# Optimization experiments

Measured on AMD Instinct MI355X. Metric: run time of the kernel, lower is better.

Reference implementation:

```python
import jax, jax.numpy as jnp
import numpy as np

_LOG2PI = 0.9189385332046727
_NUM_VARS = 256   # D
_NUM_UNITS = 64   # K
_BATCH = 2048     # B
_NUM_LEVELS = 8   # log2(D)


def setup_inputs() -> dict:
    key = jax.random.key(0)
    D, K, B = _NUM_VARS, _NUM_UNITS, _BATCH
    inp = {}
    inp["x"] = jax.random.normal(jax.random.fold_in(key, 0), (B, 1, D), dtype=jnp.float32)
    inp["mu"] = jax.random.normal(jax.random.fold_in(key, 1), (D, K), dtype=jnp.float32)
    inp["log_sigma"] = 0.1 * jax.random.normal(jax.random.fold_in(key, 2), (D, K), dtype=jnp.float32)
    # input-layer bookkeeping: each fold reads one (permuted) variable of x
    inp["in_scope_idx"] = jax.random.permutation(jax.random.fold_in(key, 3), D)[:, None]
    F = D
    for l in range(1, _NUM_LEVELS + 1):
        # fold bookkeeping: irregular pairing of previous-layer folds (permutation -> valid partition)
        inp[f"fold_idx{l}"] = jax.random.permutation(jax.random.fold_in(key, 10 + l), F).reshape(F // 2, 2)
        F //= 2
        inp[f"w{l}"] = jax.random.normal(jax.random.fold_in(key, 100 + l), (F, K, K), dtype=jnp.float32)
    return inp


def _circuit(x, mu, log_sigma, ws, in_scope_idx, fold_idxs):
    # input layer gather: x (B,C,D) -> x[..., idx] (B,C,F,s) -> permute (F,C,B,s)
    xg = jnp.transpose(x[..., in_scope_idx], (2, 1, 0, 3))  # (D,1,B,1)
    xv = xg[:, 0, :, 0]  # (D,B): C=1, scope size 1
    # Gaussian input layer, log densities: (F=D, B, K)
    z = (xv[:, :, None] - mu[:, None, :]) * jnp.exp(-log_sigma)[:, None, :]
    out = -0.5 * z * z - log_sigma[:, None, :] - _LOG2PI
    for fidx, w in zip(fold_idxs, ws):
        # folded Hadamard product layer: gather (F,2,B,K) via bookkeeping, add in log-space
        h = out[fidx].sum(axis=1)  # (F,B,K)
        # folded dense sum layer: y[f,b,j] = logsumexp_k( log softmax(w)[f,j,k] + h[f,b,k] )
        wp = jax.nn.softmax(w, axis=-1)  # (F,K,K)
        m = jnp.max(h, axis=-1, keepdims=True)
        out = jnp.log(jnp.einsum('fbk,fjk->fbj', jnp.exp(h - m), wp)) + m  # (F,B,K)
    # final bookkeeping: (F_out=1, B, K) -> transpose(0,1) -> (B, 1, K)
    return jnp.transpose(out, (1, 0, 2))


def reference(x, mu, log_sigma, w1, w2, w3, w4, w5, w6, w7, w8,
              in_scope_idx, fold_idx1, fold_idx2, fold_idx3, fold_idx4,
              fold_idx5, fold_idx6, fold_idx7, fold_idx8):
    ws = (w1, w2, w3, w4, w5, w6, w7, w8)
    fold_idxs = (fold_idx1, fold_idx2, fold_idx3, fold_idx4,
                 fold_idx5, fold_idx6, fold_idx7, fold_idx8)
    return _circuit(x, mu, log_sigma, ws, in_scope_idx, fold_idxs)
```

## Files before the change

kernel.cpp:

```cpp
#include <hip/hip_runtime.h>
#include <math.h>

#define LOG2PI_F  0.9189385332046727f
#define INV_LN2_F 1.4426950408889634f
#define LN2_F     0.6931471805599453f
#define SROW      72

typedef short bf16x8 __attribute__((ext_vector_type(8)));
typedef float f32x4  __attribute__((ext_vector_type(4)));

struct __align__(16) Op { int w; int c0; int c1; int pad; };

#define WS_WBJ   0u
#define WS_A     2097152u
#define WS_B     2162688u
#define WS_C     2228224u
#define WS_XT    2293760u
#define WS_SCHED 4390912u
#define WS_L4A   4395008u
#define WS_L4M   8589312u

__device__ __forceinline__ short bfr(float f) {
    unsigned int u = __float_as_uint(f);
    u += 0x7fffu + ((u >> 16) & 1u);
    return (short)(u >> 16);
}

__device__ __forceinline__ unsigned pk2(float a, float b) {
    return (unsigned)(unsigned short)bfr(a) | ((unsigned)(unsigned short)bfr(b) << 16);
}

struct F8v { float v[8]; };
__device__ __forceinline__ F8v ld8(const float* p) {
    F8v r;
    float4 a = *(const float4*)p;
    float4 b = *(const float4*)(p + 4);
    r.v[0]=a.x; r.v[1]=a.y; r.v[2]=a.z; r.v[3]=a.w;
    r.v[4]=b.x; r.v[5]=b.y; r.v[6]=b.z; r.v[7]=b.w;
    return r;
}

__device__ __forceinline__ void up8(int4 v, float* o) {
    o[0] = __uint_as_float(((unsigned)v.x) << 16);
    o[1] = __uint_as_float(((unsigned)v.x) & 0xffff0000u);
    o[2] = __uint_as_float(((unsigned)v.y) << 16);
    o[3] = __uint_as_float(((unsigned)v.y) & 0xffff0000u);
    o[4] = __uint_as_float(((unsigned)v.z) << 16);
    o[5] = __uint_as_float(((unsigned)v.z) & 0xffff0000u);
    o[6] = __uint_as_float(((unsigned)v.w) << 16);
    o[7] = __uint_as_float(((unsigned)v.w) & 0xffff0000u);
}

__device__ __forceinline__ float rmax16(const float hv[16]) {
    float m01 = fmaxf(hv[0], hv[1]),  m23 = fmaxf(hv[2], hv[3]);
    float m45 = fmaxf(hv[4], hv[5]),  m67 = fmaxf(hv[6], hv[7]);
    float m89 = fmaxf(hv[8], hv[9]),  mab = fmaxf(hv[10], hv[11]);
    float mcd = fmaxf(hv[12], hv[13]), mef = fmaxf(hv[14], hv[15]);
    float hm = fmaxf(fmaxf(fmaxf(m01, m23), fmaxf(m45, m67)),
                     fmaxf(fmaxf(m89, mab), fmaxf(mcd, mef)));
    hm = fmaxf(hm, __shfl_xor(hm, 16, 64));
    hm = fmaxf(hm, __shfl_xor(hm, 32, 64));
    return hm;
}

__device__ __forceinline__ void pack_p(const float e[16], bf16x8& a0, bf16x8& a1) {
    int4 p0, p1;
    p0.x = __builtin_amdgcn_perm(__float_as_uint(e[1]),  __float_as_uint(e[0]),  0x07060302u);
    p0.y = __builtin_amdgcn_perm(__float_as_uint(e[3]),  __float_as_uint(e[2]),  0x07060302u);
    p0.z = __builtin_amdgcn_perm(__float_as_uint(e[5]),  __float_as_uint(e[4]),  0x07060302u);
    p0.w = __builtin_amdgcn_perm(__float_as_uint(e[7]),  __float_as_uint(e[6]),  0x07060302u);
    p1.x = __builtin_amdgcn_perm(__float_as_uint(e[9]),  __float_as_uint(e[8]),  0x07060302u);
    p1.y = __builtin_amdgcn_perm(__float_as_uint(e[11]), __float_as_uint(e[10]), 0x07060302u);
    p1.z = __builtin_amdgcn_perm(__float_as_uint(e[13]), __float_as_uint(e[12]), 0x07060302u);
    p1.w = __builtin_amdgcn_perm(__float_as_uint(e[15]), __float_as_uint(e[14]), 0x07060302u);
    a0 = *(bf16x8*)&p0;
    a1 = *(bf16x8*)&p1;
}

__global__ __launch_bounds__(256) void prep_kernel(
    const float* __restrict__ w1, const float* __restrict__ w2,
    const float* __restrict__ w3, const float* __restrict__ w4,
    const float* __restrict__ w5, const float* __restrict__ w6,
    const float* __restrict__ w7, const float* __restrict__ w8,
    const float* __restrict__ mu, const float* __restrict__ ls,
    const float* __restrict__ x,  const int* __restrict__ scope,
    const int* __restrict__ f1, const int* __restrict__ f2,
    const int* __restrict__ f3, const int* __restrict__ f4,
    const int* __restrict__ f5, const int* __restrict__ f6,
    const int* __restrict__ f7, const int* __restrict__ f8,
    char* __restrict__ ws)
{
    const int bx = blockIdx.x, t = threadIdx.x;
    if (bx < 255) {
        const int g = bx;
        const float* src;
        if (g < 128)      src = w1 + g * 4096;
        else if (g < 192) src = w2 + (g - 128) * 4096;
        else if (g < 224) src = w3 + (g - 192) * 4096;
        else if (g < 240) src = w4 + (g - 224) * 4096;
        else if (g < 248) src = w5 + (g - 240) * 4096;
        else if (g < 252) src = w6 + (g - 248) * 4096;
        else              src = (g < 254) ? (w7 + (g - 252) * 4096) : w8;

        const int row = t >> 2;
        const int sub = t & 3;
        const float* rp = src + row * 64 + sub * 16;
        float4 v0 = *(const float4*)rp;
        float4 v1 = *(const float4*)(rp + 4);
        float4 v2 = *(const float4*)(rp + 8);
        float4 v3 = *(const float4*)(rp + 12);
        float v[16] = { v0.x, v0.y, v0.z, v0.w,  v1.x, v1.y, v1.z, v1.w,
                        v2.x, v2.y, v2.z, v2.w,  v3.x, v3.y, v3.z, v3.w };
        float mx = fmaxf(fmaxf(fmaxf(fmaxf(v[0], v[1]), fmaxf(v[2], v[3])),
                               fmaxf(fmaxf(v[4], v[5]), fmaxf(v[6], v[7]))),
                         fmaxf(fmaxf(fmaxf(v[8], v[9]), fmaxf(v[10], v[11])),
                               fmaxf(fmaxf(v[12], v[13]), fmaxf(v[14], v[15]))));
        mx = fmaxf(mx, __shfl_xor(mx, 1, 64));
        mx = fmaxf(mx, __shfl_xor(mx, 2, 64));
        float e[16], sm = 0.f;
        #pragma unroll
        for (int i = 0; i < 16; ++i) { e[i] = __expf(v[i] - mx); sm += e[i]; }
        sm += __shfl_xor(sm, 1, 64);
        sm += __shfl_xor(sm, 2, 64);
        const float inv = 1.0f / sm;

        unsigned short* dst = (unsigned short*)(ws + WS_WBJ) + g * 4096;
        #pragma unroll
        for (int c = 0; c < 2; ++c) {
            const int tc = 2 * sub + c;
            const int f  = ((row >> 4) << 1) | (tc >> 2);
            const int ln = ((tc & 3) << 4) | (row & 15);
            int4 pk;
            pk.x = (int)pk2(e[c*8+0] * inv, e[c*8+1] * inv);
            pk.y = (int)pk2(e[c*8+2] * inv, e[c*8+3] * inv);
            pk.z = (int)pk2(e[c*8+4] * inv, e[c*8+5] * inv);
            pk.w = (int)pk2(e[c*8+6] * inv, e[c*8+7] * inv);
            *(int4*)(dst + (size_t)(f * 64 + ln) * 8) = pk;
        }
    } else if (bx < 319) {
        const int idx = (bx - 255) * 256 + t;
        float m = mu[idx], l = ls[idx];
        float is2 = __expf(-2.0f * l);
        ((float*)(ws + WS_A))[idx] = -0.5f * is2 * INV_LN2_F;
        ((float*)(ws + WS_B))[idx] = m * is2 * INV_LN2_F;
        ((float*)(ws + WS_C))[idx] = (-0.5f * m * m * is2 - l - LOG2PI_F) * INV_LN2_F;
    } else if (bx < 575) {
        const int bb = bx - 319;
        const int sd = scope[t];
        float* xT = (float*)(ws + WS_XT);
        #pragma unroll
        for (int i = 0; i < 8; ++i) {
            int b = bb * 8 + i;
            xT[t * 2048 + b] = x[b * 256 + sd];
        }
    } else {
        __shared__ int sf[512];
        for (int i = t; i < 256; i += 256) sf[i]        = f1[i];
        for (int i = t; i < 128; i += 256) sf[256 + i]  = f2[i];
        for (int i = t; i <  64; i += 256) sf[384 + i]  = f3[i];
        for (int i = t; i <  32; i += 256) sf[448 + i]  = f4[i];
        for (int i = t; i <  16; i += 256) sf[480 + i]  = f5[i];
        for (int i = t; i <   8; i += 256) sf[496 + i]  = f6[i];
        for (int i = t; i <   4; i += 256) sf[504 + i]  = f7[i];
        for (int i = t; i <   2; i += 256) sf[508 + i]  = f8[i];
        __syncthreads();
        const int* F1 = &sf[0];   const int* F2 = &sf[256];
        const int* F3 = &sf[384]; const int* F4 = &sf[448];
        const int* F5 = &sf[480]; const int* F6 = &sf[496];
        const int* F7 = &sf[504]; const int* F8 = &sf[508];
        Op* base = (Op*)(ws + WS_SCHED);
        if (t < 16) {
            Op* o = base + t * 15;
            int r0 = F4[2*t], r1 = F4[2*t+1];
            int P[4] = { F3[2*r0], F3[2*r0+1], F3[2*r1], F3[2*r1+1] };
            #pragma unroll
            for (int j = 0; j < 4; ++j) {
                int L0 = F2[2*P[j]], L1 = F2[2*P[j]+1];
                o[2*j]   = { L0 * 4096, F1[2*L0], F1[2*L0+1], 0 };
                o[2*j+1] = { L1 * 4096, F1[2*L1], F1[2*L1+1], 0 };
                o[8+j]   = { (128 + P[j]) * 4096, 0, 0, 0 };
            }
            o[12] = { (192 + r0) * 4096, 0, 0, 0 };
            o[13] = { (192 + r1) * 4096, 0, 0, 0 };
            o[14] = { (224 + t)  * 4096, 0, 0, 0 };
        } else if (t == 16) {
            Op* o = base + 240;
            int g[4] = { F7[2*F8[0]], F7[2*F8[0]+1], F7[2*F8[1]], F7[2*F8[1]+1] };
            #pragma unroll
            for (int a = 0; a < 4; ++a) {
                int l0 = F6[2*g[a]], l1 = F6[2*g[a]+1];
                o[2*a]   = { (240 + l0) * 4096, F5[2*l0], F5[2*l0+1], 0 };
                o[2*a+1] = { (240 + l1) * 4096, F5[2*l1], F5[2*l1+1], 0 };
                o[8+a]   = { (248 + g[a]) * 4096, 0, 0, 0 };
            }
            o[12] = { (252 + F8[0]) * 4096, 0, 0, 0 };
            o[13] = { (252 + F8[1]) * 4096, 0, 0, 0 };
            o[14] = { 254 * 4096, 0, 0, 0 };
        }
    }
}

__device__ __forceinline__ void load_bfrag(const unsigned short* __restrict__ wbJ,
                                           int w, int lane, int4 bf[8]) {
    const int4* wp = (const int4*)(wbJ + w);
    #pragma unroll
    for (int f = 0; f < 8; ++f) bf[f] = wp[f * 64 + lane];
}

__device__ __forceinline__ void prod_norm(const float av[16], const float bv[16],
                                          float MA, float MB,
                                          float p[16], float& Mrow) {
    float pv[16];
    #pragma unroll
    for (int i = 0; i < 16; ++i) pv[i] = av[i] * bv[i];
    const float rm = rmax16(pv);
    const int e = (int)((__float_as_uint(rm) >> 23) & 0xFF) - 127;
    #pragma unroll
    for (int i = 0; i < 16; ++i) p[i] = ldexpf(pv[i], -e);
    Mrow = MA + MB + (float)e;
}

__device__ __forceinline__ void gauss_p(const Op& op,
    const float* __restrict__ xT, const float* __restrict__ Ag,
    const float* __restrict__ Bg, const float* __restrict__ Cg,
    int rowStart, int m, int q, float p[16], float& Mrow)
{
    const int d0 = op.c0, d1 = op.c1;
    const float xv0 = xT[d0 * 2048 + rowStart + m];
    const float xv1 = xT[d1 * 2048 + rowStart + m];
    const float x0s = xv0 * xv0, x1s = xv1 * xv1;
    float hv[16];
    #pragma unroll
    for (int kh = 0; kh < 2; ++kh) {
        const int kb = kh * 32 + q * 8;
        F8v A0 = ld8(Ag + d0*64 + kb), B0 = ld8(Bg + d0*64 + kb);
        F8v C0 = ld8(Cg + d0*64 + kb);
        F8v A1 = ld8(Ag + d1*64 + kb), B1 = ld8(Bg + d1*64 + kb);
        F8v C1 = ld8(Cg + d1*64 + kb);
        #pragma unroll
        for (int i = 0; i < 8; ++i) {
            float t0 = fmaf(A0.v[i], x0s, C0.v[i]);
            t0 = fmaf(B0.v[i], xv0, t0);
            float t1 = fmaf(A1.v[i], x1s, C1.v[i]);
            t1 = fmaf(B1.v[i], xv1, t1);
            hv[kh*8+i] = t0 + t1;
        }
    }
    const float hm = rmax16(hv);
    #pragma unroll
    for (int i = 0; i < 16; ++i) p[i] = __builtin_amdgcn_exp2f(hv[i] - hm);
    Mrow = hm;
}

__device__ __forceinline__ void gprod_p(const Op& op,
    const unsigned short* __restrict__ inAcc, const float* __restrict__ inM,
    int rowStart, int m, int q, float p[16], float& Mrow)
{
    const int4* A4 = (const int4*)(inAcc + (size_t)(op.c0 * 2048 + rowStart + m) * 64);
    const int4* B4 = (const int4*)(inAcc + (size_t)(op.c1 * 2048 + rowStart + m) * 64);
    float av[16], bv[16];
    up8(A4[q], av); up8(A4[4+q], av + 8);
    up8(B4[q], bv); up8(B4[4+q], bv + 8);
    prod_norm(av, bv, inM[op.c0 * 2048 + rowStart + m],
              inM[op.c1 * 2048 + rowStart + m], p, Mrow);
}

__device__ __forceinline__ void slot_prod(const unsigned short* slotS, const float* Mslot,
                                          int sA, int sB, int rowBase, int m, int q,
                                          float p[16], float& Mrow)
{
    const int4* A4 = (const int4*)(slotS + sA * 32 * SROW + (rowBase + m) * SROW);
    const int4* B4 = (const int4*)(slotS + sB * 32 * SROW + (rowBase + m) * SROW);
    float av[16], bv[16];
    up8(A4[q], av); up8(A4[4+q], av + 8);
    up8(B4[q], bv); up8(B4[4+q], bv + 8);
    prod_norm(av, bv, Mslot[sA * 32 + rowBase + m],
              Mslot[sB * 32 + rowBase + m], p, Mrow);
}

__device__ __forceinline__ void mfma8(const float p[16], const int4 bf[8], f32x4 acc[4]) {
    bf16x8 a0, a1;
    pack_p(p, a0, a1);
    #pragma unroll
    for (int jt = 0; jt < 4; ++jt) {
        f32x4 z = {0.f, 0.f, 0.f, 0.f};
        z = __builtin_amdgcn_mfma_f32_16x16x32_bf16(a0, *(bf16x8*)&bf[jt*2+0], z, 0, 0, 0);
        z = __builtin_amdgcn_mfma_f32_16x16x32_bf16(a1, *(bf16x8*)&bf[jt*2+1], z, 0, 0, 0);
        acc[jt] = z;
    }
}

__device__ __forceinline__ void store_slot(unsigned short* slotS, float* Mslot,
                                           int sl, int rowBase, const f32x4 acc[4],
                                           float Mrow, int m, int q)
{
    unsigned short* S = slotS + sl * 32 * SROW;
    #pragma unroll
    for (int jt = 0; jt < 4; ++jt)
        #pragma unroll
        for (int r = 0; r < 4; ++r)
            S[(rowBase + q*4 + r) * SROW + jt*16 + m] = (unsigned short)bfr(acc[jt][r]);
    if (q == 0) Mslot[sl * 32 + rowBase + m] = Mrow;
}

__device__ __forceinline__ void wave_fence() {
    __builtin_amdgcn_wave_barrier();
    __builtin_amdgcn_s_waitcnt(0xC07F);
    __builtin_amdgcn_wave_barrier();
}

template<int NH>
__device__ __forceinline__ void mix_core(const int4 bf[8],
    unsigned short* slotS, float* Mslot,
    int sA, int sB, int sD, int m, int q)
{
    if constexpr (NH == 2) {
        float p0[16], p1[16], M0, M1;
        slot_prod(slotS, Mslot, sA, sB, 0,  m, q, p0, M0);
        slot_prod(slotS, Mslot, sA, sB, 16, m, q, p1, M1);
        f32x4 acc0[4], acc1[4];
        mfma8(p0, bf, acc0);
        mfma8(p1, bf, acc1);
        store_slot(slotS, Mslot, sD, 0,  acc0, M0, m, q);
        store_slot(slotS, Mslot, sD, 16, acc1, M1, m, q);
    } else {
        float p[16], M;
        slot_prod(slotS, Mslot, sA, sB, 0, m, q, p, M);
        f32x4 acc[4];
        mfma8(p, bf, acc);
        store_slot(slotS, Mslot, sD, 0, acc, M, m, q);
    }
}

template<int MODE>
__global__ __launch_bounds__(256) void circuit_coop(
    const unsigned short* __restrict__ wbJ,
    const Op* __restrict__ schedG, int ntile,
    const float* __restrict__ xT, const float* __restrict__ Ag,
    const float* __restrict__ Bg, const float* __restrict__ Cg,
    const unsigned short* __restrict__ inAcc, const float* __restrict__ inM,
    unsigned short* __restrict__ outAcc, float* __restrict__ outM,
    float* __restrict__ outLog)
{
    constexpr int NH = (MODE == 0) ? 2 : 1;
    __shared__ __align__(16) unsigned short slotS[8 * 32 * SROW];
    __shared__ float Mslot[8 * 32];
    __shared__ Op ops[16];

    const int t    = threadIdx.x;
    const int wv   = t >> 6;
    const int lane = t & 63;
    const int m    = lane & 15;
    const int q    = lane >> 4;
    const int s    = blockIdx.x / ntile;
    const int b0   = (blockIdx.x % ntile) * (16 * NH);

    if (t < 15) *(int4*)&ops[t] = ((const int4*)(schedG + s * 15))[t];
    __syncthreads();

    int4 bf2[8];
    load_bfrag(wbJ, ops[8 + wv].w, lane, bf2);

    #pragma unroll
    for (int i = 0; i < 2; ++i) {
        const int sl = 2 * wv + i;
        const Op op = ops[sl];
        int4 bf[8];
        load_bfrag(wbJ, op.w, lane, bf);
        if constexpr (NH == 2) {
            float p0[16], p1[16], M0, M1;
            if (MODE == 0) {
                gauss_p(op, xT, Ag, Bg, Cg, b0,      m, q, p0, M0);
                gauss_p(op, xT, Ag, Bg, Cg, b0 + 16, m, q, p1, M1);
            } else {
                gprod_p(op, inAcc, inM, b0,      m, q, p0, M0);
                gprod_p(op, inAcc, inM, b0 + 16, m, q, p1, M1);
            }
            f32x4 acc0[4], acc1[4];
            mfma8(p0, bf, acc0);
            mfma8(p1, bf, acc1);
            store_slot(slotS, Mslot, sl, 0,  acc0, M0, m, q);
            store_slot(slotS, Mslot, sl, 16, acc1, M1, m, q);
        } else {
            float p[16], M;
            if (MODE == 0) gauss_p(op, xT, Ag, Bg, Cg, b0, m, q, p, M);
            else           gprod_p(op, inAcc, inM, b0, m, q, p, M);
            f32x4 acc[4];
            mfma8(p, bf, acc);
            store_slot(slotS, Mslot, sl, 0, acc, M, m, q);
        }
    }
    wave_fence();

    const int u = wv >> 1;
    int4 bf3[8];
    if ((wv & 1) == 0) load_bfrag(wbJ, ops[12 + u].w, lane, bf3);

    mix_core<NH>(bf2, slotS, Mslot, 2*wv, 2*wv + 1, 2*wv, m, q);
    __syncthreads();

    int4 bf4[8];
    if ((wv & 1) == 0) {
        if (wv == 0) load_bfrag(wbJ, ops[14].w, lane, bf4);
        mix_core<NH>(bf3, slotS, Mslot, 4*u, 4*u + 2, 4*u, m, q);
    }
    __syncthreads();

    if (wv == 0) {
        if constexpr (NH == 2) {
            float p0[16], p1[16], M0, M1;
            slot_prod(slotS, Mslot, 0, 4, 0,  m, q, p0, M0);
            slot_prod(slotS, Mslot, 0, 4, 16, m, q, p1, M1);
            f32x4 acc0[4], acc1[4];
            mfma8(p0, bf4, acc0);
            mfma8(p1, bf4, acc1);
            const int rowOff = s * 2048 + b0;
            #pragma unroll
            for (int jt = 0; jt < 4; ++jt)
                #pragma unroll
                for (int r = 0; r < 4; ++r) {
                    outAcc[(size_t)(rowOff +      q*4 + r) * 64 + jt*16 + m] =
                        (unsigned short)bfr(acc0[jt][r]);
                    outAcc[(size_t)(rowOff + 16 + q*4 + r) * 64 + jt*16 + m] =
                        (unsigned short)bfr(acc1[jt][r]);
                }
            if (q == 0) {
                outM[rowOff + m]      = M0;
                outM[rowOff + 16 + m] = M1;
            }
        } else {
            float p0[16], M0;
            slot_prod(slotS, Mslot, 0, 4, 0, m, q, p0, M0);
            f32x4 acc0[4];
            mfma8(p0, bf4, acc0);
            float mr0[4];
            #pragma unroll
            for (int r = 0; r < 4; ++r) mr0[r] = __shfl(M0, q * 4 + r, 64);
            #pragma unroll
            for (int jt = 0; jt < 4; ++jt)
                #pragma unroll
                for (int r = 0; r < 4; ++r)
                    outLog[(b0 + q*4 + r) * 64 + jt*16 + m] =
                        (__builtin_amdgcn_logf(acc0[jt][r]) + mr0[r]) * LN2_F;
        }
    }
}

extern "C" void kernel_launch(void* const* d_in, const int* in_sizes, int n_in,
                              void* d_out, int out_size, void* d_ws, size_t ws_size,
                              hipStream_t stream) {
    const float* x     = (const float*)d_in[0];
    const float* mu    = (const float*)d_in[1];
    const float* lsg   = (const float*)d_in[2];
    const int*   scope = (const int*)d_in[3];
    const int*   f1 = (const int*)d_in[4];   const float* w1 = (const float*)d_in[5];
    const int*   f2 = (const int*)d_in[6];   const float* w2 = (const float*)d_in[7];
    const int*   f3 = (const int*)d_in[8];   const float* w3 = (const float*)d_in[9];
    const int*   f4 = (const int*)d_in[10];  const float* w4 = (const float*)d_in[11];
    const int*   f5 = (const int*)d_in[12];  const float* w5 = (const float*)d_in[13];
    const int*   f6 = (const int*)d_in[14];  const float* w6 = (const float*)d_in[15];
    const int*   f7 = (const int*)d_in[16];  const float* w7 = (const float*)d_in[17];
    const int*   f8 = (const int*)d_in[18];  const float* w8 = (const float*)d_in[19];

    char* ws = (char*)d_ws;
    const unsigned short* wbJ = (const unsigned short*)(ws + WS_WBJ);
    const float* Ag  = (const float*)(ws + WS_A);
    const float* Bg  = (const float*)(ws + WS_B);
    const float* Cg  = (const float*)(ws + WS_C);
    const float* xT  = (const float*)(ws + WS_XT);
    const Op*    sch = (const Op*)(ws + WS_SCHED);
    unsigned short* L4A = (unsigned short*)(ws + WS_L4A);
    float*          L4M = (float*)(ws + WS_L4M);

    prep_kernel<<<576, 256, 0, stream>>>(w1, w2, w3, w4, w5, w6, w7, w8,
                                         mu, lsg, x, scope,
                                         f1, f2, f3, f4, f5, f6, f7, f8, ws);

    circuit_coop<0><<<1024, 256, 0, stream>>>(
        wbJ, sch, 64,
        xT, Ag, Bg, Cg,
        nullptr, nullptr,
        L4A, L4M, nullptr);

    circuit_coop<1><<<128, 256, 0, stream>>>(
        wbJ, sch + 240, 128,
        nullptr, nullptr, nullptr, nullptr,
        L4A, L4M,
        nullptr, nullptr, (float*)d_out);
}
```

Measured before the change: 129.6 us.

## Use 512-thread blocks so each wave computes one leaf slot

Doubles the block size from 4 to 8 waves. Each wave now handles a single first-level slot instead of looping over two, and the per-wave fence is replaced by a block-wide barrier before the mixing stages. The aim is more parallelism and less serial work per wave in the first stage. In exchange, the later stages leave more waves idle and need a full block barrier, and larger blocks may lower the number of resident blocks per CU.

```diff
diff --git a/kernel.cpp b/kernel.cpp
--- a/kernel.cpp
+++ b/kernel.cpp
@@ -303,12 +303,6 @@
     if (q == 0) Mslot[sl * 32 + rowBase + m] = Mrow;
 }
 
-__device__ __forceinline__ void wave_fence() {
-    __builtin_amdgcn_wave_barrier();
-    __builtin_amdgcn_s_waitcnt(0xC07F);
-    __builtin_amdgcn_wave_barrier();
-}
-
 template<int NH>
 __device__ __forceinline__ void mix_core(const int4 bf[8],
     unsigned short* slotS, float* Mslot,
@@ -333,7 +327,7 @@
 }
 
 template<int MODE>
-__global__ __launch_bounds__(256) void circuit_coop(
+__global__ __launch_bounds__(512) void circuit_coop(
     const unsigned short* __restrict__ wbJ,
     const Op* __restrict__ schedG, int ntile,
     const float* __restrict__ xT, const float* __restrict__ Ag,
@@ -359,12 +353,10 @@
     __syncthreads();
 
     int4 bf2[8];
-    load_bfrag(wbJ, ops[8 + wv].w, lane, bf2);
-
-    #pragma unroll
-    for (int i = 0; i < 2; ++i) {
-        const int sl = 2 * wv + i;
-        const Op op = ops[sl];
+    if (wv < 4) load_bfrag(wbJ, ops[8 + wv].w, lane, bf2);
+
+    {
+        const Op op = ops[wv];
         int4 bf[8];
         load_bfrag(wbJ, op.w, lane, bf);
         if constexpr (NH == 2) {
@@ -379,31 +371,28 @@
             f32x4 acc0[4], acc1[4];
             mfma8(p0, bf, acc0);
             mfma8(p1, bf, acc1);
-            store_slot(slotS, Mslot, sl, 0,  acc0, M0, m, q);
-            store_slot(slotS, Mslot, sl, 16, acc1, M1, m, q);
+            store_slot(slotS, Mslot, wv, 0,  acc0, M0, m, q);
+            store_slot(slotS, Mslot, wv, 16, acc1, M1, m, q);
         } else {
             float p[16], M;
             if (MODE == 0) gauss_p(op, xT, Ag, Bg, Cg, b0, m, q, p, M);
             else           gprod_p(op, inAcc, inM, b0, m, q, p, M);
             f32x4 acc[4];
             mfma8(p, bf, acc);
-            store_slot(slotS, Mslot, sl, 0, acc, M, m, q);
-        }
-    }
-    wave_fence();
-
-    const int u = wv >> 1;
+            store_slot(slotS, Mslot, wv, 0, acc, M, m, q);
+        }
+    }
+    __syncthreads();
+
     int4 bf3[8];
-    if ((wv & 1) == 0) load_bfrag(wbJ, ops[12 + u].w, lane, bf3);
-
-    mix_core<NH>(bf2, slotS, Mslot, 2*wv, 2*wv + 1, 2*wv, m, q);
+    if (wv < 2) load_bfrag(wbJ, ops[12 + wv].w, lane, bf3);
+
+    if (wv < 4) mix_core<NH>(bf2, slotS, Mslot, 2*wv, 2*wv + 1, 2*wv, m, q);
     __syncthreads();
 
     int4 bf4[8];
-    if ((wv & 1) == 0) {
-        if (wv == 0) load_bfrag(wbJ, ops[14].w, lane, bf4);
-        mix_core<NH>(bf3, slotS, Mslot, 4*u, 4*u + 2, 4*u, m, q);
-    }
+    if (wv == 0) load_bfrag(wbJ, ops[14].w, lane, bf4);
+    if (wv < 2) mix_core<NH>(bf3, slotS, Mslot, 4*wv, 4*wv + 2, 4*wv, m, q);
     __syncthreads();
 
     if (wv == 0) {
@@ -476,13 +465,13 @@
                                          mu, lsg, x, scope,
                                          f1, f2, f3, f4, f5, f6, f7, f8, ws);
 
-    circuit_coop<0><<<1024, 256, 0, stream>>>(
+    circuit_coop<0><<<1024, 512, 0, stream>>>(
         wbJ, sch, 64,
         xT, Ag, Bg, Cg,
         nullptr, nullptr,
         L4A, L4M, nullptr);
 
-    circuit_coop<1><<<128, 256, 0, stream>>>(
+    circuit_coop<1><<<128, 512, 0, stream>>>(
         wbJ, sch + 240, 128,
         nullptr, nullptr, nullptr, nullptr,
         L4A, L4M,
```

Result: slower. 135.8 us (+4.8%).
